# Kernel optimization log

Measured on AMD Instinct MI355X. Metric: run time of the kernel, lower is better.

The kernel has to match this reference:

```python
import jax, jax.numpy as jnp
import numpy as np

B, N, D_IN, D_HID, D_OUT = 8, 4096, 64, 128, 64
NEG = -1e16


def setup_inputs() -> dict:
    key = jax.random.key(0)
    k1, k2, k3, k4, k5, k6 = jax.random.split(key, 6)
    flow_x = jax.random.normal(k1, (B, N, D_IN), dtype=jnp.float32)
    adj = (jax.random.uniform(k2, (N, N)) < 0.02).astype(jnp.float32)
    graph = adj.at[jnp.arange(N), jnp.arange(N)].set(1.0)
    W1 = jax.random.normal(k3, (D_HID, D_IN), dtype=jnp.float32)
    b1 = jax.random.normal(k4, (D_HID,), dtype=jnp.float32)
    W2 = jax.random.normal(k5, (D_OUT, D_HID), dtype=jnp.float32)
    b2 = jax.random.normal(k6, (D_OUT,), dtype=jnp.float32)
    return {"flow_x": flow_x, "graph": graph, "W1": W1, "b1": b1, "W2": W2, "b2": b2}


def _gat_layer(x, graph, W, b):
    # h = Linear(x) with weight [out,in], no bias
    h = jnp.einsum('bnd,hd->bnh', x, W)
    # dense masked attention scores [B,N,N]
    s = jnp.einsum('bnh,bmh->bnm', h, h) * graph[None]
    s = jnp.where(s == 0.0, NEG, s)  # masked_fill of zeros (torch semantics)
    a = jax.nn.softmax(s, axis=2)
    return jnp.einsum('bnm,bmh->bnh', a, h) + b


def reference(flow_x, graph, W1, b1, W2, b2):
    out = _gat_layer(flow_x, graph, W1, b1)
    out = jax.nn.relu(out)
    out = _gat_layer(out, graph, W2, b2)
    return out[:, :, None, :]  # unsqueeze(2) -> [B, N, 1, D_OUT]
```

## Files before the change

kernel.cpp:

```cpp
#include <hip/hip_runtime.h>
#include <hip/hip_bf16.h>
#include <cmath>

#define B_   8
#define N_   4096
#define DIN1 64
#define DHID 128
#define DOUT2 64
#define MAXDEG 256

template <int SH>
__device__ __forceinline__ float dpp_shr_add(float p) {
    int t = __builtin_amdgcn_update_dpp(0, __float_as_int(p),
                                        0x110 | SH, 0xF, 0xF, true);
    return p + __int_as_float(t);
}
template <int GRPL>
__device__ __forceinline__ float dpp_reduce(float p) {
    if constexpr (GRPL == 16) p = dpp_shr_add<8>(p);
    p = dpp_shr_add<4>(p);
    p = dpp_shr_add<2>(p);
    p = dpp_shr_add<1>(p);
    return p;
}

__global__ __launch_bounds__(256) void k_build_csr(
    const float* __restrict__ graph, int* __restrict__ cnt, int* __restrict__ idx)
{
    const int wave = threadIdx.x >> 6;
    const int lane = threadIdx.x & 63;
    const int n = blockIdx.x * 4 + wave;
    const unsigned long long below_mask = (1ULL << lane) - 1ULL;

    const float4* __restrict__ row4 = (const float4*)(graph + (size_t)n * N_);
    int* __restrict__ myidx = idx + (size_t)n * MAXDEG;

    int base = 0;
    for (int it = 0; it < N_ / 256; ++it) {
        const int i4 = it * 64 + lane;
        float4 g = row4[i4];
        const int e = 4 * i4;
#pragma unroll
        for (int c = 0; c < 4; ++c) {
            const float gc = (c == 0) ? g.x : (c == 1) ? g.y : (c == 2) ? g.z : g.w;
            const unsigned long long mk = __ballot(gc != 0.0f);
            const int pos = base + __popcll(mk & below_mask);
            if (gc != 0.0f && pos < MAXDEG) myidx[pos] = e + c;
            base += __popcll(mk);
        }
    }
    if (lane == 0) cnt[n] = (base < MAXDEG) ? base : MAXDEG;
}

template <int DIN, int DOUT>
__global__ __launch_bounds__(256) void k_linear(
    const float* __restrict__ x, const float* __restrict__ W,
    float* __restrict__ out)
{
    constexpr int CG = DOUT / 4;
    constexpr int RG = 256 / CG;
    constexpr int TR = 32 / RG;

    __shared__ float sWt[DIN][DOUT + 4];

    const int t = threadIdx.x;
    const float4* W4 = (const float4*)W;
    for (int i = t; i < DOUT * (DIN / 4); i += 256) {
        int kk = i / (DIN / 4);
        int d4 = i % (DIN / 4);
        float4 w = W4[i];
        sWt[4 * d4 + 0][kk] = w.x;
        sWt[4 * d4 + 1][kk] = w.y;
        sWt[4 * d4 + 2][kk] = w.z;
        sWt[4 * d4 + 3][kk] = w.w;
    }
    __syncthreads();

    const int rg = t / CG;
    const int c  = t % CG;
    const int base = blockIdx.x * 32;
    const float4* x4 = (const float4*)x;

    float acc[TR][4];
#pragma unroll
    for (int i = 0; i < TR; ++i)
#pragma unroll
        for (int j = 0; j < 4; ++j) acc[i][j] = 0.0f;

    for (int d4 = 0; d4 < DIN / 4; ++d4) {
        float4 xf[TR];
#pragma unroll
        for (int i = 0; i < TR; ++i)
            xf[i] = x4[(size_t)(base + rg * TR + i) * (DIN / 4) + d4];
        float4 wf[4];
#pragma unroll
        for (int dd = 0; dd < 4; ++dd)
            wf[dd] = *(const float4*)&sWt[4 * d4 + dd][4 * c];
#pragma unroll
        for (int i = 0; i < TR; ++i) {
            acc[i][0] += xf[i].x * wf[0].x + xf[i].y * wf[1].x + xf[i].z * wf[2].x + xf[i].w * wf[3].x;
            acc[i][1] += xf[i].x * wf[0].y + xf[i].y * wf[1].y + xf[i].z * wf[2].y + xf[i].w * wf[3].y;
            acc[i][2] += xf[i].x * wf[0].z + xf[i].y * wf[1].z + xf[i].z * wf[2].z + xf[i].w * wf[3].z;
            acc[i][3] += xf[i].x * wf[0].w + xf[i].y * wf[1].w + xf[i].z * wf[2].w + xf[i].w * wf[3].w;
        }
    }

#pragma unroll
    for (int i = 0; i < TR; ++i) {
        float4 o = {acc[i][0], acc[i][1], acc[i][2], acc[i][3]};
        ((float4*)out)[(size_t)(base + rg * TR + i) * CG + c] = o;
    }
}

template <int D, bool RELU>
__global__ __launch_bounds__(256) void k_attn(
    const float* __restrict__ h, const int* __restrict__ cnt,
    const int* __restrict__ idx, const float* __restrict__ bias,
    float* __restrict__ out)
{
    constexpr int V    = D / 4;
    constexpr int GRPL = (D == 128) ? 16 : 8;
    constexpr int GS   = 64 / GRPL;
    constexpr int NF   = V / GRPL;
    constexpr int RB   = D * 4;
    const unsigned long long TOPMASK =
        (GRPL == 16) ? 0x8000800080008000ULL : 0x8080808080808080ULL;

    const int bid  = blockIdx.x;
    const int b    = bid & 7;
    const int wave = threadIdx.x >> 6;
    const int lane = threadIdx.x & 63;
    const int n    = (bid >> 3) * 4 + wave;
    const int grp  = lane / GRPL;
    const int gl   = lane % GRPL;
    const int gtop = lane | (GRPL - 1);

    __shared__ int s_off[4][MAXDEG + 16];

    const int k = cnt[n];
    const int* __restrict__ myidx = idx + (size_t)n * MAXDEG;
    for (int j = lane; j < k; j += 64) s_off[wave][j] = myidx[j] * RB;
    if (lane < 16) s_off[wave][k + lane] = 0;

    const char* __restrict__ hb = (const char*)h + (size_t)b * N_ * RB;
    const int lb = gl * 16;

    float4 qf[NF];
#pragma unroll
    for (int i = 0; i < NF; ++i)
        qf[i] = *(const float4*)(hb + (size_t)n * RB + lb + GRPL * 16 * i);

    float m;
    {
        float p = 0.0f;
#pragma unroll
        for (int i = 0; i < NF; ++i)
            p += qf[i].x * qf[i].x + qf[i].y * qf[i].y
               + qf[i].z * qf[i].z + qf[i].w * qf[i].w;
        p = dpp_reduce<GRPL>(p);
        const float pb = __shfl(p, gtop, 64);
        m = (pb != 0.0f) ? pb : -INFINITY;
    }
    float mt = m - 100.0f;
    float s = 0.0f;
    float4 acc[NF];
#pragma unroll
    for (int i = 0; i < NF; ++i) acc[i] = {0.0f, 0.0f, 0.0f, 0.0f};

    auto loadrow = [&](float4 (&r)[NF], int j) {
        const char* hm = hb + s_off[wave][j];
#pragma unroll
        for (int i = 0; i < NF; ++i)
            r[i] = *(const float4*)(hm + lb + GRPL * 16 * i);
    };
    auto process = [&](const float4 (&cur)[NF]) {
        float p = 0.0f;
#pragma unroll
        for (int i = 0; i < NF; ++i)
            p += qf[i].x * cur[i].x + qf[i].y * cur[i].y
               + qf[i].z * cur[i].z + qf[i].w * cur[i].w;
        p = dpp_reduce<GRPL>(p);
        if (__builtin_expect((__ballot(p > mt) & TOPMASK) != 0ULL, 0)) {
            const float pb = __shfl(p, gtop, 64);
            const bool valid = (pb != 0.0f);
            const float pm   = valid ? pb : m;
            const float newm = fmaxf(m, pm);
            const float f = (m == newm) ? 1.0f : __expf(m - newm);
            const float e = valid ? __expf(pb - newm) : 0.0f;
            s = s * f + e;
#pragma unroll
            for (int i = 0; i < NF; ++i) {
                acc[i].x = acc[i].x * f + e * cur[i].x;
                acc[i].y = acc[i].y * f + e * cur[i].y;
                acc[i].z = acc[i].z * f + e * cur[i].z;
                acc[i].w = acc[i].w * f + e * cur[i].w;
            }
            m = newm;
            mt = m - 100.0f;
        }
    };

    {
        float4 r0[NF], r1[NF], r2[NF];
        loadrow(r0, grp);
        loadrow(r1, grp + GS);
        int j = grp;
        while (j < k) {
            loadrow(r2, j + 2 * GS);
            process(r0);
            j += GS; if (j >= k) break;
            loadrow(r0, j + 2 * GS);
            process(r1);
            j += GS; if (j >= k) break;
            loadrow(r1, j + 2 * GS);
            process(r2);
            j += GS;
        }
    }

#pragma unroll
    for (int mask = GRPL; mask <= 32; mask <<= 1) {
        const float m2 = __shfl_xor(m, mask, 64);
        const float s2 = __shfl_xor(s, mask, 64);
        float4 a2[NF];
#pragma unroll
        for (int i = 0; i < NF; ++i) {
            a2[i].x = __shfl_xor(acc[i].x, mask, 64);
            a2[i].y = __shfl_xor(acc[i].y, mask, 64);
            a2[i].z = __shfl_xor(acc[i].z, mask, 64);
            a2[i].w = __shfl_xor(acc[i].w, mask, 64);
        }
        const float mm = fmaxf(m, m2);
        const float f1 = (m  == mm) ? 1.0f : __expf(m  - mm);
        const float f2 = (m2 == mm) ? 1.0f : __expf(m2 - mm);
        s = s * f1 + s2 * f2;
#pragma unroll
        for (int i = 0; i < NF; ++i) {
            acc[i].x = acc[i].x * f1 + a2[i].x * f2;
            acc[i].y = acc[i].y * f1 + a2[i].y * f2;
            acc[i].z = acc[i].z * f1 + a2[i].z * f2;
            acc[i].w = acc[i].w * f1 + a2[i].w * f2;
        }
        m = mm;
    }

    if (s > 0.0f) {
        if (grp == 0) {
            const float4* bias4 = (const float4*)bias;
            const float inv = 1.0f / s;
#pragma unroll
            for (int i = 0; i < NF; ++i) {
                const float4 bi = bias4[gl + GRPL * i];
                float4 o;
                o.x = acc[i].x * inv + bi.x;
                o.y = acc[i].y * inv + bi.y;
                o.z = acc[i].z * inv + bi.z;
                o.w = acc[i].w * inv + bi.w;
                if (RELU) {
                    o.x = fmaxf(o.x, 0.0f); o.y = fmaxf(o.y, 0.0f);
                    o.z = fmaxf(o.z, 0.0f); o.w = fmaxf(o.w, 0.0f);
                }
                ((float4*)out)[((size_t)b * N_ + n) * V + gl + GRPL * i] = o;
            }
        }
    } else {
        const float4* hb4 = (const float4*)hb;
        constexpr int RS = 64 / V;
        const int sl = lane % V;
        const int rs = lane / V;
        float4 a = {0.0f, 0.0f, 0.0f, 0.0f};
        for (int row = rs; row < N_; row += RS) {
            float4 v = hb4[(size_t)row * V + sl];
            a.x += v.x; a.y += v.y; a.z += v.z; a.w += v.w;
        }
#pragma unroll
        for (int mask = V; mask < 64; mask <<= 1) {
            a.x += __shfl_xor(a.x, mask, 64);
            a.y += __shfl_xor(a.y, mask, 64);
            a.z += __shfl_xor(a.z, mask, 64);
            a.w += __shfl_xor(a.w, mask, 64);
        }
        if (lane < V) {
            constexpr float invN = 1.0f / (float)N_;
            const float4 bi = ((const float4*)bias)[sl];
            float4 o;
            o.x = a.x * invN + bi.x;
            o.y = a.y * invN + bi.y;
            o.z = a.z * invN + bi.z;
            o.w = a.w * invN + bi.w;
            if (RELU) {
                o.x = fmaxf(o.x, 0.0f); o.y = fmaxf(o.y, 0.0f);
                o.z = fmaxf(o.z, 0.0f); o.w = fmaxf(o.w, 0.0f);
            }
            ((float4*)out)[((size_t)b * N_ + n) * V + sl] = o;
        }
    }
}

extern "C" void kernel_launch(void* const* d_in, const int* in_sizes, int n_in,
                              void* d_out, int out_size, void* d_ws, size_t ws_size,
                              hipStream_t stream) {
    (void)in_sizes; (void)n_in; (void)out_size; (void)ws_size;

    const float* flow_x = (const float*)d_in[0];
    const float* graph  = (const float*)d_in[1];
    const float* W1     = (const float*)d_in[2];
    const float* b1     = (const float*)d_in[3];
    const float* W2     = (const float*)d_in[4];
    const float* b2     = (const float*)d_in[5];
    float* out = (float*)d_out;

    char* p = (char*)d_ws;
    auto carve = [&](size_t bytes) -> void* {
        void* r = (void*)p;
        p += (bytes + 255) & ~(size_t)255;
        return r;
    };
    int*   nbr_cnt = (int*)carve((size_t)N_ * sizeof(int));
    int*   nbr_idx = (int*)carve((size_t)N_ * MAXDEG * sizeof(int));
    float* h1      = (float*)carve((size_t)B_ * N_ * DHID * sizeof(float));
    float* x2      = (float*)carve((size_t)B_ * N_ * DHID * sizeof(float));
    float* h2      = (float*)carve((size_t)B_ * N_ * DOUT2 * sizeof(float));

    k_build_csr<<<N_ / 4, 256, 0, stream>>>(graph, nbr_cnt, nbr_idx);

    k_linear<DIN1, DHID><<<(B_ * N_) / 32, 256, 0, stream>>>(flow_x, W1, h1);

    k_attn<DHID, true><<<N_ * B_ / 4, 256, 0, stream>>>(h1, nbr_cnt, nbr_idx, b1, x2);

    k_linear<DHID, DOUT2><<<(B_ * N_) / 32, 256, 0, stream>>>(x2, W2, h2);

    k_attn<DOUT2, false><<<N_ * B_ / 4, 256, 0, stream>>>(h2, nbr_cnt, nbr_idx, b2, out);
}
```

Measured before the change: 270.2 us.

## Fuse CSR build with first linear and fuse second linear into attention

Merges the CSR-building kernel and the first linear projection into one launch, with block ranges split by block index so the two independent jobs run side by side. Fuses the second linear layer into the first attention kernel: the ReLU output row goes to shared memory and each lane computes one output channel from W2 read from global memory. This removes the x2 intermediate buffer round trip and two kernel launches. In exchange the attention kernel gains a barrier and per-row W2 reads, which rely on caching.

```diff
diff --git a/kernel.cpp b/kernel.cpp
--- a/kernel.cpp
+++ b/kernel.cpp
@@ -24,46 +24,45 @@
     return p;
 }
 
-__global__ __launch_bounds__(256) void k_build_csr(
-    const float* __restrict__ graph, int* __restrict__ cnt, int* __restrict__ idx)
-{
-    const int wave = threadIdx.x >> 6;
-    const int lane = threadIdx.x & 63;
-    const int n = blockIdx.x * 4 + wave;
-    const unsigned long long below_mask = (1ULL << lane) - 1ULL;
-
-    const float4* __restrict__ row4 = (const float4*)(graph + (size_t)n * N_);
-    int* __restrict__ myidx = idx + (size_t)n * MAXDEG;
-
-    int base = 0;
-    for (int it = 0; it < N_ / 256; ++it) {
-        const int i4 = it * 64 + lane;
-        float4 g = row4[i4];
-        const int e = 4 * i4;
-#pragma unroll
-        for (int c = 0; c < 4; ++c) {
-            const float gc = (c == 0) ? g.x : (c == 1) ? g.y : (c == 2) ? g.z : g.w;
-            const unsigned long long mk = __ballot(gc != 0.0f);
-            const int pos = base + __popcll(mk & below_mask);
-            if (gc != 0.0f && pos < MAXDEG) myidx[pos] = e + c;
-            base += __popcll(mk);
-        }
-    }
-    if (lane == 0) cnt[n] = (base < MAXDEG) ? base : MAXDEG;
-}
-
 template <int DIN, int DOUT>
-__global__ __launch_bounds__(256) void k_linear(
+__global__ __launch_bounds__(256) void k_csr_linear(
+    const float* __restrict__ graph, int* __restrict__ cnt, int* __restrict__ idx,
     const float* __restrict__ x, const float* __restrict__ W,
     float* __restrict__ out)
 {
+    __shared__ float sWt[DIN][DOUT + 4];
+    const int t = threadIdx.x;
+
+    if (blockIdx.x < N_ / 4) {
+        const int wave = t >> 6;
+        const int lane = t & 63;
+        const int n = blockIdx.x * 4 + wave;
+        const unsigned long long below_mask = (1ULL << lane) - 1ULL;
+        const float4* __restrict__ row4 = (const float4*)(graph + (size_t)n * N_);
+        int* __restrict__ myidx = idx + (size_t)n * MAXDEG;
+        int base = 0;
+        for (int it = 0; it < N_ / 256; ++it) {
+            const int i4 = it * 64 + lane;
+            float4 g = row4[i4];
+            const int e = 4 * i4;
+#pragma unroll
+            for (int c = 0; c < 4; ++c) {
+                const float gc = (c == 0) ? g.x : (c == 1) ? g.y : (c == 2) ? g.z : g.w;
+                const unsigned long long mk = __ballot(gc != 0.0f);
+                const int pos = base + __popcll(mk & below_mask);
+                if (gc != 0.0f && pos < MAXDEG) myidx[pos] = e + c;
+                base += __popcll(mk);
+            }
+        }
+        if (lane == 0) cnt[n] = (base < MAXDEG) ? base : MAXDEG;
+        return;
+    }
+
     constexpr int CG = DOUT / 4;
     constexpr int RG = 256 / CG;
     constexpr int TR = 32 / RG;
-
-    __shared__ float sWt[DIN][DOUT + 4];
-
-    const int t = threadIdx.x;
+    const int lb = blockIdx.x - N_ / 4;
+
     const float4* W4 = (const float4*)W;
     for (int i = t; i < DOUT * (DIN / 4); i += 256) {
         int kk = i / (DIN / 4);
@@ -78,7 +77,7 @@
 
     const int rg = t / CG;
     const int c  = t % CG;
-    const int base = blockIdx.x * 32;
+    const int base = lb * 32;
     const float4* x4 = (const float4*)x;
 
     float acc[TR][4];
@@ -104,7 +103,6 @@
             acc[i][3] += xf[i].x * wf[0].w + xf[i].y * wf[1].w + xf[i].z * wf[2].w + xf[i].w * wf[3].w;
         }
     }
-
 #pragma unroll
     for (int i = 0; i < TR; ++i) {
         float4 o = {acc[i][0], acc[i][1], acc[i][2], acc[i][3]};
@@ -112,30 +110,27 @@
     }
 }
 
-template <int D, bool RELU>
-__global__ __launch_bounds__(256) void k_attn(
+__global__ __launch_bounds__(256) void k_attn1_lin2(
     const float* __restrict__ h, const int* __restrict__ cnt,
     const int* __restrict__ idx, const float* __restrict__ bias,
-    float* __restrict__ out)
+    const float* __restrict__ W2, float* __restrict__ h2out)
 {
-    constexpr int V    = D / 4;
-    constexpr int GRPL = (D == 128) ? 16 : 8;
-    constexpr int GS   = 64 / GRPL;
-    constexpr int NF   = V / GRPL;
-    constexpr int RB   = D * 4;
-    const unsigned long long TOPMASK =
-        (GRPL == 16) ? 0x8000800080008000ULL : 0x8080808080808080ULL;
+    constexpr int D  = DHID;
+    constexpr int V  = D / 4;
+    constexpr int NF = 2;
+    constexpr int RB = D * 4;
 
     const int bid  = blockIdx.x;
     const int b    = bid & 7;
     const int wave = threadIdx.x >> 6;
     const int lane = threadIdx.x & 63;
     const int n    = (bid >> 3) * 4 + wave;
-    const int grp  = lane / GRPL;
-    const int gl   = lane % GRPL;
-    const int gtop = lane | (GRPL - 1);
-
-    __shared__ int s_off[4][MAXDEG + 16];
+    const int grp  = lane >> 4;
+    const int gl   = lane & 15;
+    const int gtop = lane | 15;
+
+    __shared__ int   s_off[4][MAXDEG + 16];
+    __shared__ float s_x2[4][DHID];
 
     const int k = cnt[n];
     const int* __restrict__ myidx = idx + (size_t)n * MAXDEG;
@@ -148,7 +143,7 @@
     float4 qf[NF];
 #pragma unroll
     for (int i = 0; i < NF; ++i)
-        qf[i] = *(const float4*)(hb + (size_t)n * RB + lb + GRPL * 16 * i);
+        qf[i] = *(const float4*)(hb + (size_t)n * RB + lb + 256 * i);
 
     float m;
     {
@@ -157,7 +152,7 @@
         for (int i = 0; i < NF; ++i)
             p += qf[i].x * qf[i].x + qf[i].y * qf[i].y
                + qf[i].z * qf[i].z + qf[i].w * qf[i].w;
-        p = dpp_reduce<GRPL>(p);
+        p = dpp_reduce<16>(p);
         const float pb = __shfl(p, gtop, 64);
         m = (pb != 0.0f) ? pb : -INFINITY;
     }
@@ -170,8 +165,7 @@
     auto loadrow = [&](float4 (&r)[NF], int j) {
         const char* hm = hb + s_off[wave][j];
 #pragma unroll
-        for (int i = 0; i < NF; ++i)
-            r[i] = *(const float4*)(hm + lb + GRPL * 16 * i);
+        for (int i = 0; i < NF; ++i) r[i] = *(const float4*)(hm + lb + 256 * i);
     };
     auto process = [&](const float4 (&cur)[NF]) {
         float p = 0.0f;
@@ -179,8 +173,8 @@
         for (int i = 0; i < NF; ++i)
             p += qf[i].x * cur[i].x + qf[i].y * cur[i].y
                + qf[i].z * cur[i].z + qf[i].w * cur[i].w;
-        p = dpp_reduce<GRPL>(p);
-        if (__builtin_expect((__ballot(p > mt) & TOPMASK) != 0ULL, 0)) {
+        p = dpp_reduce<16>(p);
+        if (__builtin_expect((__ballot(p > mt) & 0x8000800080008000ULL) != 0ULL, 0)) {
             const float pb = __shfl(p, gtop, 64);
             const bool valid = (pb != 0.0f);
             const float pm   = valid ? pb : m;
@@ -203,23 +197,23 @@
     {
         float4 r0[NF], r1[NF], r2[NF];
         loadrow(r0, grp);
-        loadrow(r1, grp + GS);
+        loadrow(r1, grp + 4);
         int j = grp;
         while (j < k) {
-            loadrow(r2, j + 2 * GS);
+            loadrow(r2, j + 8);
             process(r0);
-            j += GS; if (j >= k) break;
-            loadrow(r0, j + 2 * GS);
+            j += 4; if (j >= k) break;
+            loadrow(r0, j + 8);
             process(r1);
-            j += GS; if (j >= k) break;
-            loadrow(r1, j + 2 * GS);
+            j += 4; if (j >= k) break;
+            loadrow(r1, j + 8);
             process(r2);
-            j += GS;
-        }
-    }
-
-#pragma unroll
-    for (int mask = GRPL; mask <= 32; mask <<= 1) {
+            j += 4;
+        }
+    }
+
+#pragma unroll
+    for (int mask = 16; mask <= 32; mask <<= 1) {
         const float m2 = __shfl_xor(m, mask, 64);
         const float s2 = __shfl_xor(s, mask, 64);
         float4 a2[NF];
@@ -250,31 +244,209 @@
             const float inv = 1.0f / s;
 #pragma unroll
             for (int i = 0; i < NF; ++i) {
-                const float4 bi = bias4[gl + GRPL * i];
+                const float4 bi = bias4[gl + 16 * i];
+                float4 o;
+                o.x = fmaxf(acc[i].x * inv + bi.x, 0.0f);
+                o.y = fmaxf(acc[i].y * inv + bi.y, 0.0f);
+                o.z = fmaxf(acc[i].z * inv + bi.z, 0.0f);
+                o.w = fmaxf(acc[i].w * inv + bi.w, 0.0f);
+                *(float4*)&s_x2[wave][4 * (gl + 16 * i)] = o;
+            }
+        }
+    } else {
+        const float4* hb4 = (const float4*)hb;
+        const int sl = lane % V;
+        const int rs = lane / V;
+        float4 a = {0.0f, 0.0f, 0.0f, 0.0f};
+        for (int row = rs; row < N_; row += 2) {
+            float4 v = hb4[(size_t)row * V + sl];
+            a.x += v.x; a.y += v.y; a.z += v.z; a.w += v.w;
+        }
+        a.x += __shfl_xor(a.x, 32, 64);
+        a.y += __shfl_xor(a.y, 32, 64);
+        a.z += __shfl_xor(a.z, 32, 64);
+        a.w += __shfl_xor(a.w, 32, 64);
+        if (lane < V) {
+            constexpr float invN = 1.0f / (float)N_;
+            const float4 bi = ((const float4*)bias)[sl];
+            float4 o;
+            o.x = fmaxf(a.x * invN + bi.x, 0.0f);
+            o.y = fmaxf(a.y * invN + bi.y, 0.0f);
+            o.z = fmaxf(a.z * invN + bi.z, 0.0f);
+            o.w = fmaxf(a.w * invN + bi.w, 0.0f);
+            *(float4*)&s_x2[wave][4 * sl] = o;
+        }
+    }
+    __syncthreads();
+
+    {
+        const float4* w2r = (const float4*)(W2 + (size_t)lane * DHID);
+        const float4* xr  = (const float4*)&s_x2[wave][0];
+        float a0 = 0.0f, a1 = 0.0f;
+#pragma unroll
+        for (int d4 = 0; d4 < DHID / 8; ++d4) {
+            float4 xv0 = xr[2 * d4],     wv0 = w2r[2 * d4];
+            float4 xv1 = xr[2 * d4 + 1], wv1 = w2r[2 * d4 + 1];
+            a0 += xv0.x * wv0.x + xv0.y * wv0.y + xv0.z * wv0.z + xv0.w * wv0.w;
+            a1 += xv1.x * wv1.x + xv1.y * wv1.y + xv1.z * wv1.z + xv1.w * wv1.w;
+        }
+        h2out[((size_t)b * N_ + n) * DOUT2 + lane] = a0 + a1;
+    }
+}
+
+__global__ __launch_bounds__(256) void k_attn2(
+    const float* __restrict__ h, const int* __restrict__ cnt,
+    const int* __restrict__ idx, const float* __restrict__ bias,
+    float* __restrict__ out)
+{
+    constexpr int D  = DOUT2;
+    constexpr int V  = D / 4;
+    constexpr int NF = 2;
+    constexpr int RB = D * 4;
+
+    const int bid  = blockIdx.x;
+    const int b    = bid & 7;
+    const int wave = threadIdx.x >> 6;
+    const int lane = threadIdx.x & 63;
+    const int n    = (bid >> 3) * 4 + wave;
+    const int grp  = lane >> 3;
+    const int gl   = lane & 7;
+    const int gtop = lane | 7;
+
+    __shared__ int s_off[4][MAXDEG + 16];
+
+    const int k = cnt[n];
+    const int* __restrict__ myidx = idx + (size_t)n * MAXDEG;
+    for (int j = lane; j < k; j += 64) s_off[wave][j] = myidx[j] * RB;
+    if (lane < 16) s_off[wave][k + lane] = 0;
+
+    const char* __restrict__ hb = (const char*)h + (size_t)b * N_ * RB;
+    const int lb = gl * 16;
+
+    float4 qf[NF];
+#pragma unroll
+    for (int i = 0; i < NF; ++i)
+        qf[i] = *(const float4*)(hb + (size_t)n * RB + lb + 128 * i);
+
+    float m;
+    {
+        float p = 0.0f;
+#pragma unroll
+        for (int i = 0; i < NF; ++i)
+            p += qf[i].x * qf[i].x + qf[i].y * qf[i].y
+               + qf[i].z * qf[i].z + qf[i].w * qf[i].w;
+        p = dpp_reduce<8>(p);
+        const float pb = __shfl(p, gtop, 64);
+        m = (pb != 0.0f) ? pb : -INFINITY;
+    }
+    float mt = m - 100.0f;
+    float s = 0.0f;
+    float4 acc[NF];
+#pragma unroll
+    for (int i = 0; i < NF; ++i) acc[i] = {0.0f, 0.0f, 0.0f, 0.0f};
+
+    auto loadrow = [&](float4 (&r)[NF], int j) {
+        const char* hm = hb + s_off[wave][j];
+#pragma unroll
+        for (int i = 0; i < NF; ++i) r[i] = *(const float4*)(hm + lb + 128 * i);
+    };
+    auto process = [&](const float4 (&cur)[NF]) {
+        float p = 0.0f;
+#pragma unroll
+        for (int i = 0; i < NF; ++i)
+            p += qf[i].x * cur[i].x + qf[i].y * cur[i].y
+               + qf[i].z * cur[i].z + qf[i].w * cur[i].w;
+        p = dpp_reduce<8>(p);
+        if (__builtin_expect((__ballot(p > mt) & 0x8080808080808080ULL) != 0ULL, 0)) {
+            const float pb = __shfl(p, gtop, 64);
+            const bool valid = (pb != 0.0f);
+            const float pm   = valid ? pb : m;
+            const float newm = fmaxf(m, pm);
+            const float f = (m == newm) ? 1.0f : __expf(m - newm);
+            const float e = valid ? __expf(pb - newm) : 0.0f;
+            s = s * f + e;
+#pragma unroll
+            for (int i = 0; i < NF; ++i) {
+                acc[i].x = acc[i].x * f + e * cur[i].x;
+                acc[i].y = acc[i].y * f + e * cur[i].y;
+                acc[i].z = acc[i].z * f + e * cur[i].z;
+                acc[i].w = acc[i].w * f + e * cur[i].w;
+            }
+            m = newm;
+            mt = m - 100.0f;
+        }
+    };
+
+    {
+        float4 r0[NF], r1[NF], r2[NF];
+        loadrow(r0, grp);
+        loadrow(r1, grp + 8);
+        int j = grp;
+        while (j < k) {
+            loadrow(r2, j + 16);
+            process(r0);
+            j += 8; if (j >= k) break;
+            loadrow(r0, j + 16);
+            process(r1);
+            j += 8; if (j >= k) break;
+            loadrow(r1, j + 16);
+            process(r2);
+            j += 8;
+        }
+    }
+
+#pragma unroll
+    for (int mask = 8; mask <= 32; mask <<= 1) {
+        const float m2 = __shfl_xor(m, mask, 64);
+        const float s2 = __shfl_xor(s, mask, 64);
+        float4 a2[NF];
+#pragma unroll
+        for (int i = 0; i < NF; ++i) {
+            a2[i].x = __shfl_xor(acc[i].x, mask, 64);
+            a2[i].y = __shfl_xor(acc[i].y, mask, 64);
+            a2[i].z = __shfl_xor(acc[i].z, mask, 64);
+            a2[i].w = __shfl_xor(acc[i].w, mask, 64);
+        }
+        const float mm = fmaxf(m, m2);
+        const float f1 = (m  == mm) ? 1.0f : __expf(m  - mm);
+        const float f2 = (m2 == mm) ? 1.0f : __expf(m2 - mm);
+        s = s * f1 + s2 * f2;
+#pragma unroll
+        for (int i = 0; i < NF; ++i) {
+            acc[i].x = acc[i].x * f1 + a2[i].x * f2;
+            acc[i].y = acc[i].y * f1 + a2[i].y * f2;
+            acc[i].z = acc[i].z * f1 + a2[i].z * f2;
+            acc[i].w = acc[i].w * f1 + a2[i].w * f2;
+        }
+        m = mm;
+    }
+
+    if (s > 0.0f) {
+        if (grp == 0) {
+            const float4* bias4 = (const float4*)bias;
+            const float inv = 1.0f / s;
+#pragma unroll
+            for (int i = 0; i < NF; ++i) {
+                const float4 bi = bias4[gl + 8 * i];
                 float4 o;
                 o.x = acc[i].x * inv + bi.x;
                 o.y = acc[i].y * inv + bi.y;
                 o.z = acc[i].z * inv + bi.z;
                 o.w = acc[i].w * inv + bi.w;
-                if (RELU) {
-                    o.x = fmaxf(o.x, 0.0f); o.y = fmaxf(o.y, 0.0f);
-                    o.z = fmaxf(o.z, 0.0f); o.w = fmaxf(o.w, 0.0f);
-                }
-                ((float4*)out)[((size_t)b * N_ + n) * V + gl + GRPL * i] = o;
+                ((float4*)out)[((size_t)b * N_ + n) * V + gl + 8 * i] = o;
             }
         }
     } else {
         const float4* hb4 = (const float4*)hb;
-        constexpr int RS = 64 / V;
         const int sl = lane % V;
         const int rs = lane / V;
         float4 a = {0.0f, 0.0f, 0.0f, 0.0f};
-        for (int row = rs; row < N_; row += RS) {
+        for (int row = rs; row < N_; row += 4) {
             float4 v = hb4[(size_t)row * V + sl];
             a.x += v.x; a.y += v.y; a.z += v.z; a.w += v.w;
         }
 #pragma unroll
-        for (int mask = V; mask < 64; mask <<= 1) {
+        for (int mask = 16; mask <= 32; mask <<= 1) {
             a.x += __shfl_xor(a.x, mask, 64);
             a.y += __shfl_xor(a.y, mask, 64);
             a.z += __shfl_xor(a.z, mask, 64);
@@ -288,10 +460,6 @@
             o.y = a.y * invN + bi.y;
             o.z = a.z * invN + bi.z;
             o.w = a.w * invN + bi.w;
-            if (RELU) {
-                o.x = fmaxf(o.x, 0.0f); o.y = fmaxf(o.y, 0.0f);
-                o.z = fmaxf(o.z, 0.0f); o.w = fmaxf(o.w, 0.0f);
-            }
             ((float4*)out)[((size_t)b * N_ + n) * V + sl] = o;
         }
     }
@@ -319,16 +487,12 @@
     int*   nbr_cnt = (int*)carve((size_t)N_ * sizeof(int));
     int*   nbr_idx = (int*)carve((size_t)N_ * MAXDEG * sizeof(int));
     float* h1      = (float*)carve((size_t)B_ * N_ * DHID * sizeof(float));
-    float* x2      = (float*)carve((size_t)B_ * N_ * DHID * sizeof(float));
     float* h2      = (float*)carve((size_t)B_ * N_ * DOUT2 * sizeof(float));
 
-    k_build_csr<<<N_ / 4, 256, 0, stream>>>(graph, nbr_cnt, nbr_idx);
-
-    k_linear<DIN1, DHID><<<(B_ * N_) / 32, 256, 0, stream>>>(flow_x, W1, h1);
-
-    k_attn<DHID, true><<<N_ * B_ / 4, 256, 0, stream>>>(h1, nbr_cnt, nbr_idx, b1, x2);
-
-    k_linear<DHID, DOUT2><<<(B_ * N_) / 32, 256, 0, stream>>>(x2, W2, h2);
-
-    k_attn<DOUT2, false><<<N_ * B_ / 4, 256, 0, stream>>>(h2, nbr_cnt, nbr_idx, b2, out);
-}
+    k_csr_linear<DIN1, DHID><<<N_ / 4 + (B_ * N_) / 32, 256, 0, stream>>>(
+        graph, nbr_cnt, nbr_idx, flow_x, W1, h1);
+
+    k_attn1_lin2<<<N_ * B_ / 4, 256, 0, stream>>>(h1, nbr_cnt, nbr_idx, b1, W2, h2);
+
+    k_attn2<<<N_ * B_ / 4, 256, 0, stream>>>(h2, nbr_cnt, nbr_idx, b2, out);
+}
```

Result: slower. 375.9 us (+39.1%).
